# Kernel optimization log

Measured on AMD Instinct MI355X. Metric: run time of the kernel, lower is better.

Reference implementation:

```python
import jax, jax.numpy as jnp
import numpy as np

N_NODES = 50000
N_RAND_EDGES = 800000
LEAKY_SLOPE = 0.2


def gat_layer(x, edge_index, W, a_src, a_dst, b, num_heads):
    """Multi-head GAT layer. W: [Din, Dout]; heads split Dout; concat output."""
    N = x.shape[0]
    Dout = W.shape[1]
    Dh = Dout // num_heads
    z = (x @ W).reshape(N, num_heads, Dh)                      # [N,H,Dh]
    src = edge_index[0]
    dst = edge_index[1]
    alpha_src = jnp.einsum('nhd,hd->nh', z, a_src)             # [N,H]
    alpha_dst = jnp.einsum('nhd,hd->nh', z, a_dst)             # [N,H]
    e = jax.nn.leaky_relu(alpha_src[src] + alpha_dst[dst], LEAKY_SLOPE)  # [E,H]
    # segment softmax over incoming edges of each dst node
    m = jax.ops.segment_max(e, dst, num_segments=N)            # [N,H]
    e = jnp.exp(e - m[dst])
    denom = jax.ops.segment_sum(e, dst, num_segments=N)        # [N,H]
    alpha = e / (denom[dst] + 1e-16)                           # [E,H]
    msg = z[src] * alpha[:, :, None]                           # [E,H,Dh]
    out = jax.ops.segment_sum(msg, dst, num_segments=N)        # [N,H,Dh]
    return out.reshape(N, Dout) + b


def setup_inputs() -> dict:
    key = jax.random.key(0)
    ks = jax.random.split(key, 12)
    input_dim, hidden_dim, num_classes, num_heads = 128, 64, 16, 8
    x = jax.random.normal(ks[0], (N_NODES, input_dim), dtype=jnp.float32)
    rand_edges = jax.random.randint(ks[1], (2, N_RAND_EDGES), 0, N_NODES, dtype=jnp.int32)
    self_loops = jnp.tile(jnp.arange(N_NODES, dtype=jnp.int32), (2, 1))
    edge_indices = jnp.concatenate([rand_edges, self_loops], axis=1)   # [2, 850000]

    def glorot(k, shape):
        fan = sum(shape[-2:]) if len(shape) > 1 else shape[0]
        return jax.random.normal(k, shape, dtype=jnp.float32) * (2.0 / fan) ** 0.5

    W1 = glorot(ks[2], (input_dim, hidden_dim))
    a_src1 = glorot(ks[3], (num_heads, hidden_dim // num_heads))
    a_dst1 = glorot(ks[4], (num_heads, hidden_dim // num_heads))
    b1 = jnp.zeros((hidden_dim,), dtype=jnp.float32)
    W2 = glorot(ks[5], (hidden_dim, num_classes))
    a_src2 = glorot(ks[6], (1, num_classes))
    a_dst2 = glorot(ks[7], (1, num_classes))
    b2 = jnp.zeros((num_classes,), dtype=jnp.float32)
    return {"x": x, "edge_indices": edge_indices,
            "W1": W1, "a_src1": a_src1, "a_dst1": a_dst1, "b1": b1,
            "W2": W2, "a_src2": a_src2, "a_dst2": a_dst2, "b2": b2}


def reference(x, edge_indices, W1, a_src1, a_dst1, b1, W2, a_src2, a_dst2, b2):
    # Dropout is identity in eval mode.
    h = gat_layer(x, edge_indices, W1, a_src1, a_dst1, b1, num_heads=8)
    h = jax.nn.elu(h)
    return gat_layer(h, edge_indices, W2, a_src2, a_dst2, b2, num_heads=1)
```

## Files before the change

### kernel.cpp

```cpp
#include <hip/hip_runtime.h>
#include <hip/hip_fp16.h>


#define LRELU(v) ((v) > 0.f ? (v) : 0.2f * (v))

#define NB   196
#define BCAP 5120

__global__ void __launch_bounds__(256, 4)
kA(const float* __restrict__ x, const float* __restrict__ W1,
   const float* __restrict__ a_src1, const float* __restrict__ a_dst1,
   const int* __restrict__ src, const int* __restrict__ dst,
   int* __restrict__ bcnt, int* __restrict__ pairs,
   __half* __restrict__ z1h, float* __restrict__ as1,
   float* __restrict__ ad1, int N, int E) {
    __shared__ float xs[64][133];
    __shared__ float avs[128];
    int b = blockIdx.x;
    int tid = threadIdx.x;
    bool is_part = ((b % 5) == 4);

    if (is_part) {
        int* hist  = (int*)&xs[0][0];
        int* base_ = hist + 256;
        int* cur   = hist + 512;
        int rank = b / 5;
        if (tid < NB) hist[tid] = 0;
        __syncthreads();
        int chunk = (E + NB - 1) / NB;
        int e0 = rank * chunk;
        int e1 = min(e0 + chunk, E);
        for (int e = e0 + tid; e < e1; e += 256)
            atomicAdd(&hist[dst[e] >> 8], 1);
        __syncthreads();
        if (tid < NB) {
            base_[tid] = atomicAdd(&bcnt[tid], hist[tid]);
            cur[tid] = 0;
        }
        __syncthreads();
        for (int e = e0 + tid; e < e1; e += 256) {
            int d = dst[e], s = src[e];
            int bk = d >> 8;
            int r = atomicAdd(&cur[bk], 1);
            int idx = base_[bk] + r;
            if (idx < BCAP) pairs[bk * BCAP + idx] = (s << 8) | (d & 255);
        }
        return;
    }

    int tile = (b / 5) * 4 + (b % 5);
    if (tile >= 782) return;
    int n0 = tile * 64;
    for (int idx = tid; idx < 2048; idx += 256) {
        int r = idx >> 5, q = idx & 31;
        int n = n0 + r; if (n >= N) n = N - 1;
        float4 v = ((const float4*)(x + (size_t)n * 128))[q];
        *(float4*)&xs[r][q * 4] = v;
    }
    if (tid < 128) avs[tid] = (tid < 64) ? a_src1[tid] : a_dst1[tid - 64];
    __syncthreads();

    int rg = tid >> 4, cg2 = tid & 15;
    int xr = rg * 4;
    const float4* wb = (const float4*)W1 + cg2;
    float acc[4][4] = {};
    float4 xv[4], wl[4];
#pragma unroll
    for (int i = 0; i < 4; ++i) xv[i] = *(const float4*)&xs[xr + i][0];
#pragma unroll
    for (int kk = 0; kk < 4; ++kk) wl[kk] = wb[kk * 16];
#pragma unroll 2
    for (int k4 = 0; k4 < 32; ++k4) {
        float4 xn[4], wn[4];
        int kn = (k4 + 1) & 31;
#pragma unroll
        for (int i = 0; i < 4; ++i) xn[i] = *(const float4*)&xs[xr + i][kn * 4];
#pragma unroll
        for (int kk = 0; kk < 4; ++kk) wn[kk] = wb[(kn * 4 + kk) * 16];
#pragma unroll
        for (int i = 0; i < 4; ++i) {
            acc[i][0] += xv[i].x * wl[0].x; acc[i][1] += xv[i].x * wl[0].y;
            acc[i][2] += xv[i].x * wl[0].z; acc[i][3] += xv[i].x * wl[0].w;
            acc[i][0] += xv[i].y * wl[1].x; acc[i][1] += xv[i].y * wl[1].y;
            acc[i][2] += xv[i].y * wl[1].z; acc[i][3] += xv[i].y * wl[1].w;
            acc[i][0] += xv[i].z * wl[2].x; acc[i][1] += xv[i].z * wl[2].y;
            acc[i][2] += xv[i].z * wl[2].z; acc[i][3] += xv[i].z * wl[2].w;
            acc[i][0] += xv[i].w * wl[3].x; acc[i][1] += xv[i].w * wl[3].y;
            acc[i][2] += xv[i].w * wl[3].z; acc[i][3] += xv[i].w * wl[3].w;
        }
#pragma unroll
        for (int i = 0; i < 4; ++i) { xv[i] = xn[i]; wl[i] = wn[i]; }
    }
    int h = cg2 >> 1, db = (cg2 & 1) * 4;
    float pas[4], pad_[4];
#pragma unroll
    for (int i = 0; i < 4; ++i) {
        float s = 0.f, dd = 0.f;
#pragma unroll
        for (int j = 0; j < 4; ++j) {
            s  += acc[i][j] * avs[h * 8 + db + j];
            dd += acc[i][j] * avs[64 + h * 8 + db + j];
        }
        pas[i] = s; pad_[i] = dd;
    }
#pragma unroll
    for (int i = 0; i < 4; ++i) {
        pas[i]  += __shfl_xor(pas[i], 1, 64);
        pad_[i] += __shfl_xor(pad_[i], 1, 64);
    }
#pragma unroll
    for (int i = 0; i < 4; ++i) {
        int n = n0 + rg * 4 + i;
        if (n < N) {
            union { __half2 h2[2]; uint2 u; } pk;
            pk.h2[0] = __floats2half2_rn(acc[i][0], acc[i][1]);
            pk.h2[1] = __floats2half2_rn(acc[i][2], acc[i][3]);
            *(uint2*)&z1h[(size_t)n * 64 + cg2 * 4] = pk.u;
            if ((cg2 & 1) == 0) {
                as1[(size_t)n * 8 + h] = pas[i];
                ad1[(size_t)n * 8 + h] = pad_[i];
            }
        }
    }
}

__global__ void kB(const int* __restrict__ bcnt, const int* __restrict__ pairs,
                   int* __restrict__ deg, int* __restrict__ csr, int N) {
    __shared__ int cur[256];
    int b = blockIdx.x;
    int tid = threadIdx.x;
    cur[tid] = 0;
    __syncthreads();
    int nb = min(bcnt[b], BCAP);
    const int* p = pairs + b * BCAP;
    for (int i = tid; i < nb; i += 256) {
        int v = p[i];
        int off = v & 255, s = v >> 8;
        int r = atomicAdd(&cur[off], 1);
        if (r < 64) csr[(((b << 8) + off) << 6) + r] = s;
    }
    __syncthreads();
    int d = (b << 8) + tid;
    if (d < N) deg[d] = cur[tid];
}

__global__ void kg1(const int* __restrict__ deg, const int* __restrict__ csr,
                    const float* __restrict__ as1, const float* __restrict__ ad1,
                    const __half* __restrict__ z1h, const float* __restrict__ b1,
                    const float* __restrict__ W2, const float* __restrict__ a_src2,
                    const float* __restrict__ a_dst2,
                    float* __restrict__ z2, float* __restrict__ as2,
                    float* __restrict__ ad2, int N) {
    __shared__ int s_idx[4][8][65];
    __shared__ float hs[4][8][68];
    __shared__ float ws2[64][18];
    int tid = threadIdx.x;
    int lane = tid & 63, wid = tid >> 6;
    for (int i = tid; i < 1024; i += 256) ws2[i >> 4][i & 15] = W2[i];
    __syncthreads();

    int dloc = lane >> 3, q = lane & 7;
    int dbase = blockIdx.x * 32 + wid * 8;
    int d = dbase + dloc;
    int dc = d < N ? d : N - 1;
    int cnt = d < N ? min(deg[d], 64) : 0;
    for (int dd = 0; dd < 8; ++dd) {
        int dr = dbase + dd; if (dr >= N) dr = N - 1;
        int cdd = min(deg[dr], 64);
        if (lane < cdd) s_idx[wid][dd][lane] = csr[(dr << 6) + lane];
    }
    float adv = ad1[(size_t)dc * 8 + q];
    float a0 = 0.f, a1 = 0.f, a2 = 0.f, a3 = 0.f;
    float a4 = 0.f, a5 = 0.f, a6 = 0.f, a7 = 0.f, dsum = 0.f;
#pragma unroll 2
    for (int j = 0; j < cnt; ++j) {
        int s = s_idx[wid][dloc][j];
        float ev = as1[(size_t)s * 8 + q] + adv;
        float w = __expf(LRELU(ev));
        float4 raw = *(const float4*)(z1h + (size_t)s * 64 + q * 8);
        const __half2* hp = (const __half2*)&raw;
        float2 f0 = __half22float2(hp[0]), f1 = __half22float2(hp[1]);
        float2 f2 = __half22float2(hp[2]), f3 = __half22float2(hp[3]);
        a0 += w * f0.x; a1 += w * f0.y; a2 += w * f1.x; a3 += w * f1.y;
        a4 += w * f2.x; a5 += w * f2.y; a6 += w * f3.x; a7 += w * f3.y;
        dsum += w;
    }
    float inv = cnt ? 1.f / dsum : 0.f;
    float4 bv0 = *(const float4*)(b1 + q * 8);
    float4 bv1 = *(const float4*)(b1 + q * 8 + 4);
    float hv[8] = {a0 * inv + bv0.x, a1 * inv + bv0.y,
                   a2 * inv + bv0.z, a3 * inv + bv0.w,
                   a4 * inv + bv1.x, a5 * inv + bv1.y,
                   a6 * inv + bv1.z, a7 * inv + bv1.w};
#pragma unroll
    for (int i = 0; i < 8; ++i) hv[i] = hv[i] > 0.f ? hv[i] : expm1f(hv[i]);
    *(float4*)&hs[wid][dloc][q * 8]     = make_float4(hv[0], hv[1], hv[2], hv[3]);
    *(float4*)&hs[wid][dloc][q * 8 + 4] = make_float4(hv[4], hv[5], hv[6], hv[7]);
    float zc0 = 0.f, zc1 = 0.f;
#pragma unroll
    for (int k4 = 0; k4 < 16; ++k4) {
        float4 hh = *(const float4*)&hs[wid][dloc][k4 * 4];
        float2 w0 = *(const float2*)&ws2[k4 * 4 + 0][q * 2];
        float2 w1 = *(const float2*)&ws2[k4 * 4 + 1][q * 2];
        float2 w2 = *(const float2*)&ws2[k4 * 4 + 2][q * 2];
        float2 w3 = *(const float2*)&ws2[k4 * 4 + 3][q * 2];
        zc0 += hh.x * w0.x; zc1 += hh.x * w0.y;
        zc0 += hh.y * w1.x; zc1 += hh.y * w1.y;
        zc0 += hh.z * w2.x; zc1 += hh.z * w2.y;
        zc0 += hh.w * w3.x; zc1 += hh.w * w3.y;
    }
    if (d < N) *(float2*)&z2[(size_t)d * 16 + q * 2] = make_float2(zc0, zc1);
    float ps = zc0 * a_src2[q * 2] + zc1 * a_src2[q * 2 + 1];
    float pd = zc0 * a_dst2[q * 2] + zc1 * a_dst2[q * 2 + 1];
#pragma unroll
    for (int m = 1; m < 8; m <<= 1) {
        ps += __shfl_xor(ps, m, 8);
        pd += __shfl_xor(pd, m, 8);
    }
    if (q == 0 && d < N) { as2[d] = ps; ad2[d] = pd; }
}

__global__ void kg2(const int* __restrict__ deg, const int* __restrict__ csr,
                    const float* __restrict__ as2, const float* __restrict__ ad2,
                    const float* __restrict__ z2, const float* __restrict__ b2,
                    float* __restrict__ out, int N) {
    __shared__ int s_idx[4][16][65];
    int tid = threadIdx.x;
    int lane = tid & 63, wid = tid >> 6;
    int dloc = lane >> 2, c = lane & 3;
    int dbase = blockIdx.x * 64 + wid * 16;
    int d = dbase + dloc;
    int dc = d < N ? d : N - 1;
    int cnt = d < N ? min(deg[d], 64) : 0;
    for (int dd = 0; dd < 16; ++dd) {
        int dr = dbase + dd; if (dr >= N) dr = N - 1;
        int cdd = min(deg[dr], 64);
        if (lane < cdd) s_idx[wid][dd][lane] = csr[(dr << 6) + lane];
    }
    float adv = ad2[dc];
    float ax = 0.f, ay = 0.f, az = 0.f, aw = 0.f, dsum = 0.f;
#pragma unroll 2
    for (int j = 0; j < cnt; ++j) {
        int s = s_idx[wid][dloc][j];
        float ev = as2[s] + adv;
        float w = __expf(LRELU(ev));
        float4 zv = *(const float4*)(z2 + (size_t)s * 16 + c * 4);
        ax += w * zv.x; ay += w * zv.y; az += w * zv.z; aw += w * zv.w;
        dsum += w;
    }
    if (d < N) {
        float inv = 1.f / dsum;
        float4 o = make_float4(ax * inv + b2[c * 4], ay * inv + b2[c * 4 + 1],
                               az * inv + b2[c * 4 + 2], aw * inv + b2[c * 4 + 3]);
        *(float4*)&out[(size_t)d * 16 + c * 4] = o;
    }
}

extern "C" void kernel_launch(void* const* d_in, const int* in_sizes, int n_in,
                              void* d_out, int out_size, void* d_ws, size_t ws_size,
                              hipStream_t stream) {
    const float* x      = (const float*)d_in[0];
    const int*   ei     = (const int*)d_in[1];
    const float* W1     = (const float*)d_in[2];
    const float* a_src1 = (const float*)d_in[3];
    const float* a_dst1 = (const float*)d_in[4];
    const float* b1     = (const float*)d_in[5];
    const float* W2     = (const float*)d_in[6];
    const float* a_src2 = (const float*)d_in[7];
    const float* a_dst2 = (const float*)d_in[8];
    const float* b2     = (const float*)d_in[9];
    float* out = (float*)d_out;

    const int N = in_sizes[0] / 128;
    const int E = in_sizes[1] / 2;
    const int* src = ei;
    const int* dst = ei + E;

    float* ws = (float*)d_ws;
    size_t off = 0;
    __half* z1h = (__half*)(ws + off); off += (size_t)N * 32;
    float* as1 = ws + off; off += (size_t)N * 8;
    float* ad1 = ws + off; off += (size_t)N * 8;
    float* z2  = ws + off; off += (size_t)N * 16;
    float* as2 = ws + off; off += (size_t)N;
    float* ad2 = ws + off; off += (size_t)N;
    int* csr = (int*)(ws + off); off += (size_t)N * 64;
    int* deg = (int*)(ws + off); off += (size_t)N;
    int* pairs = (int*)(ws + off); off += (size_t)NB * BCAP;
    int* bcnt = (int*)(ws + off); off += NB;

    hipMemsetAsync(bcnt, 0, (size_t)NB * sizeof(int), stream);

    kA<<<980, 256, 0, stream>>>(x, W1, a_src1, a_dst1, src, dst, bcnt, pairs,
                                z1h, as1, ad1, N, E);
    kB<<<NB, 256, 0, stream>>>(bcnt, pairs, deg, csr, N);
    kg1<<<(N + 31) / 32, 256, 0, stream>>>(deg, csr, as1, ad1, z1h, b1, W2,
                                           a_src2, a_dst2, z2, as2, ad2, N);
    kg2<<<(N + 63) / 64, 256, 0, stream>>>(deg, csr, as2, ad2, z2, b2, out, N);
}
```

Baseline: 171.1 us.

## Recompute source attention scores from gathered features and pack layer-2 node records

Layer 1 no longer stores per-node source attention scores. kg1 recomputes them per edge as a dot product of the already-gathered half-precision features with a_src1, which removes one random gather per edge at the cost of eight extra FMAs. It also changes rounding, since the score now comes from fp16 features. Layer 2 packs z2, as2 and ad2 into one 32-float row per node so each edge's gather touches a single cache line, and both gather loops are unrolled 4 instead of 2.

```diff
diff --git a/kernel.cpp b/kernel.cpp
--- a/kernel.cpp
+++ b/kernel.cpp
@@ -9,13 +9,12 @@
 
 __global__ void __launch_bounds__(256, 4)
 kA(const float* __restrict__ x, const float* __restrict__ W1,
-   const float* __restrict__ a_src1, const float* __restrict__ a_dst1,
+   const float* __restrict__ a_dst1,
    const int* __restrict__ src, const int* __restrict__ dst,
    int* __restrict__ bcnt, int* __restrict__ pairs,
-   __half* __restrict__ z1h, float* __restrict__ as1,
-   float* __restrict__ ad1, int N, int E) {
+   __half* __restrict__ z1h, float* __restrict__ ad1, int N, int E) {
     __shared__ float xs[64][133];
-    __shared__ float avs[128];
+    __shared__ float avs[64];
     int b = blockIdx.x;
     int tid = threadIdx.x;
     bool is_part = ((b % 5) == 4);
@@ -57,7 +56,7 @@
         float4 v = ((const float4*)(x + (size_t)n * 128))[q];
         *(float4*)&xs[r][q * 4] = v;
     }
-    if (tid < 128) avs[tid] = (tid < 64) ? a_src1[tid] : a_dst1[tid - 64];
+    if (tid < 64) avs[tid] = a_dst1[tid];
     __syncthreads();
 
     int rg = tid >> 4, cg2 = tid & 15;
@@ -92,22 +91,17 @@
         for (int i = 0; i < 4; ++i) { xv[i] = xn[i]; wl[i] = wn[i]; }
     }
     int h = cg2 >> 1, db = (cg2 & 1) * 4;
-    float pas[4], pad_[4];
+    float pad_[4];
 #pragma unroll
     for (int i = 0; i < 4; ++i) {
-        float s = 0.f, dd = 0.f;
-#pragma unroll
-        for (int j = 0; j < 4; ++j) {
-            s  += acc[i][j] * avs[h * 8 + db + j];
-            dd += acc[i][j] * avs[64 + h * 8 + db + j];
-        }
-        pas[i] = s; pad_[i] = dd;
-    }
-#pragma unroll
-    for (int i = 0; i < 4; ++i) {
-        pas[i]  += __shfl_xor(pas[i], 1, 64);
+        float dd = 0.f;
+#pragma unroll
+        for (int j = 0; j < 4; ++j) dd += acc[i][j] * avs[h * 8 + db + j];
+        pad_[i] = dd;
+    }
+#pragma unroll
+    for (int i = 0; i < 4; ++i)
         pad_[i] += __shfl_xor(pad_[i], 1, 64);
-    }
 #pragma unroll
     for (int i = 0; i < 4; ++i) {
         int n = n0 + rg * 4 + i;
@@ -116,10 +110,7 @@
             pk.h2[0] = __floats2half2_rn(acc[i][0], acc[i][1]);
             pk.h2[1] = __floats2half2_rn(acc[i][2], acc[i][3]);
             *(uint2*)&z1h[(size_t)n * 64 + cg2 * 4] = pk.u;
-            if ((cg2 & 1) == 0) {
-                as1[(size_t)n * 8 + h] = pas[i];
-                ad1[(size_t)n * 8 + h] = pad_[i];
-            }
+            if ((cg2 & 1) == 0) ad1[(size_t)n * 8 + h] = pad_[i];
         }
     }
 }
@@ -145,12 +136,11 @@
 }
 
 __global__ void kg1(const int* __restrict__ deg, const int* __restrict__ csr,
-                    const float* __restrict__ as1, const float* __restrict__ ad1,
+                    const float* __restrict__ a_src1, const float* __restrict__ ad1,
                     const __half* __restrict__ z1h, const float* __restrict__ b1,
                     const float* __restrict__ W2, const float* __restrict__ a_src2,
                     const float* __restrict__ a_dst2,
-                    float* __restrict__ z2, float* __restrict__ as2,
-                    float* __restrict__ ad2, int N) {
+                    float* __restrict__ z2r, int N) {
     __shared__ int s_idx[4][8][65];
     __shared__ float hs[4][8][68];
     __shared__ float ws2[64][18];
@@ -170,17 +160,21 @@
         if (lane < cdd) s_idx[wid][dd][lane] = csr[(dr << 6) + lane];
     }
     float adv = ad1[(size_t)dc * 8 + q];
+    float4 asA = *(const float4*)(a_src1 + q * 8);
+    float4 asB = *(const float4*)(a_src1 + q * 8 + 4);
     float a0 = 0.f, a1 = 0.f, a2 = 0.f, a3 = 0.f;
     float a4 = 0.f, a5 = 0.f, a6 = 0.f, a7 = 0.f, dsum = 0.f;
-#pragma unroll 2
+#pragma unroll 4
     for (int j = 0; j < cnt; ++j) {
         int s = s_idx[wid][dloc][j];
-        float ev = as1[(size_t)s * 8 + q] + adv;
-        float w = __expf(LRELU(ev));
         float4 raw = *(const float4*)(z1h + (size_t)s * 64 + q * 8);
         const __half2* hp = (const __half2*)&raw;
         float2 f0 = __half22float2(hp[0]), f1 = __half22float2(hp[1]);
         float2 f2 = __half22float2(hp[2]), f3 = __half22float2(hp[3]);
+        float av = f0.x * asA.x + f0.y * asA.y + f1.x * asA.z + f1.y * asA.w
+                 + f2.x * asB.x + f2.y * asB.y + f3.x * asB.z + f3.y * asB.w;
+        float ev = av + adv;
+        float w = __expf(LRELU(ev));
         a0 += w * f0.x; a1 += w * f0.y; a2 += w * f1.x; a3 += w * f1.y;
         a4 += w * f2.x; a5 += w * f2.y; a6 += w * f3.x; a7 += w * f3.y;
         dsum += w;
@@ -209,7 +203,7 @@
         zc0 += hh.z * w2.x; zc1 += hh.z * w2.y;
         zc0 += hh.w * w3.x; zc1 += hh.w * w3.y;
     }
-    if (d < N) *(float2*)&z2[(size_t)d * 16 + q * 2] = make_float2(zc0, zc1);
+    if (d < N) *(float2*)&z2r[(size_t)d * 32 + q * 2] = make_float2(zc0, zc1);
     float ps = zc0 * a_src2[q * 2] + zc1 * a_src2[q * 2 + 1];
     float pd = zc0 * a_dst2[q * 2] + zc1 * a_dst2[q * 2 + 1];
 #pragma unroll
@@ -217,12 +211,14 @@
         ps += __shfl_xor(ps, m, 8);
         pd += __shfl_xor(pd, m, 8);
     }
-    if (q == 0 && d < N) { as2[d] = ps; ad2[d] = pd; }
+    if (q == 0 && d < N) {
+        z2r[(size_t)d * 32 + 16] = ps;
+        z2r[(size_t)d * 32 + 17] = pd;
+    }
 }
 
 __global__ void kg2(const int* __restrict__ deg, const int* __restrict__ csr,
-                    const float* __restrict__ as2, const float* __restrict__ ad2,
-                    const float* __restrict__ z2, const float* __restrict__ b2,
+                    const float* __restrict__ z2r, const float* __restrict__ b2,
                     float* __restrict__ out, int N) {
     __shared__ int s_idx[4][16][65];
     int tid = threadIdx.x;
@@ -237,14 +233,15 @@
         int cdd = min(deg[dr], 64);
         if (lane < cdd) s_idx[wid][dd][lane] = csr[(dr << 6) + lane];
     }
-    float adv = ad2[dc];
+    float adv = z2r[(size_t)dc * 32 + 17];
     float ax = 0.f, ay = 0.f, az = 0.f, aw = 0.f, dsum = 0.f;
-#pragma unroll 2
+#pragma unroll 4
     for (int j = 0; j < cnt; ++j) {
         int s = s_idx[wid][dloc][j];
-        float ev = as2[s] + adv;
+        float as2v = z2r[(size_t)s * 32 + 16];
+        float ev = as2v + adv;
         float w = __expf(LRELU(ev));
-        float4 zv = *(const float4*)(z2 + (size_t)s * 16 + c * 4);
+        float4 zv = *(const float4*)(z2r + (size_t)s * 32 + c * 4);
         ax += w * zv.x; ay += w * zv.y; az += w * zv.z; aw += w * zv.w;
         dsum += w;
     }
@@ -279,11 +276,8 @@
     float* ws = (float*)d_ws;
     size_t off = 0;
     __half* z1h = (__half*)(ws + off); off += (size_t)N * 32;
-    float* as1 = ws + off; off += (size_t)N * 8;
     float* ad1 = ws + off; off += (size_t)N * 8;
-    float* z2  = ws + off; off += (size_t)N * 16;
-    float* as2 = ws + off; off += (size_t)N;
-    float* ad2 = ws + off; off += (size_t)N;
+    float* z2r = ws + off; off += (size_t)N * 32;
     int* csr = (int*)(ws + off); off += (size_t)N * 64;
     int* deg = (int*)(ws + off); off += (size_t)N;
     int* pairs = (int*)(ws + off); off += (size_t)NB * BCAP;
@@ -291,10 +285,10 @@
 
     hipMemsetAsync(bcnt, 0, (size_t)NB * sizeof(int), stream);
 
-    kA<<<980, 256, 0, stream>>>(x, W1, a_src1, a_dst1, src, dst, bcnt, pairs,
-                                z1h, as1, ad1, N, E);
+    kA<<<980, 256, 0, stream>>>(x, W1, a_dst1, src, dst, bcnt, pairs,
+                                z1h, ad1, N, E);
     kB<<<NB, 256, 0, stream>>>(bcnt, pairs, deg, csr, N);
-    kg1<<<(N + 31) / 32, 256, 0, stream>>>(deg, csr, as1, ad1, z1h, b1, W2,
-                                           a_src2, a_dst2, z2, as2, ad2, N);
-    kg2<<<(N + 63) / 64, 256, 0, stream>>>(deg, csr, as2, ad2, z2, b2, out, N);
-}
+    kg1<<<(N + 31) / 32, 256, 0, stream>>>(deg, csr, a_src1, ad1, z1h, b1, W2,
+                                           a_src2, a_dst2, z2r, N);
+    kg2<<<(N + 63) / 64, 256, 0, stream>>>(deg, csr, z2r, b2, out, N);
+}
```

Result: no change. 171.8 us (+0.4%).
